# Kernel optimization log

Measured on AMD Instinct MI355X. Metric: run time of the kernel, lower is better.

## Reference

```python
import jax, jax.numpy as jnp
import numpy as np

NV, NQ, K, C, FF, H = 40000, 8192, 96, 128, 256, 8
DH = C // H


def _layernorm(x, g, b, eps=1e-5):
    m = jnp.mean(x, axis=-1, keepdims=True)
    v = jnp.var(x, axis=-1, keepdims=True)
    return (x - m) * jax.lax.rsqrt(v + eps) * g + b


def setup_inputs() -> dict:
    key = jax.random.key(0)
    ks = jax.random.split(key, 20)
    voxel_features = jax.random.normal(ks[0], (NV, C), dtype=jnp.float32)
    voxel_coords = jax.random.normal(ks[1], (NV, 3), dtype=jnp.float32)
    query_coords = jax.random.normal(ks[2], (NQ, 3), dtype=jnp.float32)
    raw = jax.random.randint(ks[3], (NQ, K), 0, 50000)
    key_indices = jnp.where(raw >= NV, -1, raw)  # -1 marks padded/missing keys
    key_indices = key_indices.at[:, 0].set(raw[:, 0] % NV)  # ensure >=1 valid key per query
    w = lambda k, shape: (jax.random.normal(k, shape, dtype=jnp.float32) * 0.02)
    return {
        "voxel_features": voxel_features,
        "voxel_coords": voxel_coords,
        "query_coords": query_coords,
        "key_indices": key_indices,
        "norm1_g": jnp.ones((C,), jnp.float32), "norm1_b": jnp.zeros((C,), jnp.float32),
        "q_pos_w": w(ks[4], (C, 3)), "q_pos_b": jnp.zeros((C,), jnp.float32),
        "k_pos_w": w(ks[5], (C, 3)), "k_pos_b": jnp.zeros((C,), jnp.float32),
        "in_w": w(ks[6], (3 * C, C)), "in_b": jnp.zeros((3 * C,), jnp.float32),
        "out_w": w(ks[7], (C, C)), "out_b": jnp.zeros((C,), jnp.float32),
        "norm2_g": jnp.ones((C,), jnp.float32), "norm2_b": jnp.zeros((C,), jnp.float32),
        "lin1_w": w(ks[8], (FF, C)), "lin1_b": jnp.zeros((FF,), jnp.float32),
        "lin2_w": w(ks[9], (C, FF)), "lin2_b": jnp.zeros((C,), jnp.float32),
        "fin_w": w(ks[10], (C, C)), "fin_b": jnp.zeros((C,), jnp.float32),
    }


def reference(voxel_features, voxel_coords, query_coords, key_indices,
              norm1_g, norm1_b, q_pos_w, q_pos_b, k_pos_w, k_pos_b,
              in_w, in_b, out_w, out_b, norm2_g, norm2_b,
              lin1_w, lin1_b, lin2_w, lin2_b, fin_w, fin_b):
    mask = key_indices < 0                      # [NQ, K] True = padded
    idx = jnp.where(mask, 0, key_indices)
    vf = _layernorm(voxel_features, norm1_g, norm1_b)   # norm1
    key_feat = vf[idx]                          # gather: [NQ, K, C]
    key_c = voxel_coords[idx]                   # [NQ, K, 3]
    # q_pos_proj: Linear(3,C)+ReLU ; k_pos_proj: Conv1d(3,C,1)+ReLU (== per-key linear)
    q_feat = jax.nn.relu(query_coords @ q_pos_w.T + q_pos_b)        # [NQ, C]
    key_pos = jax.nn.relu(jnp.einsum('nkt,ct->nkc', key_c, k_pos_w) + k_pos_b)
    key_feat = key_feat + key_pos               # [NQ, K, C]
    # nn.MultiheadAttention: query [1,NQ,C], key/value [K,NQ,C] -> per-query attention over K keys
    wq, wk, wv = in_w[:C], in_w[C:2 * C], in_w[2 * C:]
    bq, bk, bv = in_b[:C], in_b[C:2 * C], in_b[2 * C:]
    q = (q_feat @ wq.T + bq).reshape(NQ, H, DH)                 # [NQ,H,DH]
    k = (key_feat @ wk.T + bk).reshape(NQ, K, H, DH)            # [NQ,K,H,DH]
    v = (key_feat @ wv.T + bv).reshape(NQ, K, H, DH)
    scale = 1.0 / np.sqrt(DH)
    scores = jnp.einsum('nhd,nkhd->nhk', q, k) * scale          # [NQ,H,K]
    scores = jnp.where(mask[:, None, :], jnp.float32(-1e9), scores)
    attn = jax.nn.softmax(scores, axis=-1)
    ctx = jnp.einsum('nhk,nkhd->nhd', attn, v).reshape(NQ, C)
    attend = ctx @ out_w.T + out_b                              # [NQ,C]
    # FFN block (dropout=0 -> identity)
    h = _layernorm(attend, norm2_g, norm2_b)
    act = jax.nn.relu(h @ lin1_w.T + lin1_b) @ lin2_w.T + lin2_b
    x = attend + act
    out = jax.nn.relu(x @ fin_w.T + fin_b)                      # output_layer
    return out
```

## Files before the change

### kernel.cpp

```cpp
#include <hip/hip_runtime.h>
#include <hip/hip_bf16.h>
#include <math.h>

constexpr int NVOX = 40000;
constexpr int NQRY = 8192;
constexpr int KK   = 96;
constexpr int CH   = 128;
constexpr int FFD  = 256;

typedef __attribute__((ext_vector_type(8))) short short8;
typedef __attribute__((ext_vector_type(4))) float float4v;

__device__ inline float bflo(unsigned u) { return __uint_as_float(u << 16); }
__device__ inline float bfhi(unsigned u) { return __uint_as_float(u & 0xffff0000u); }
__device__ inline unsigned short f2bf(float x) {
  union { float f; unsigned u; } a; a.f = x;
  const unsigned r = a.u + 0x7fffu + ((a.u >> 16) & 1u);
  return (unsigned short)(r >> 16);
}
__device__ inline unsigned pack2(float lo, float hi) {
  return (unsigned)f2bf(lo) | ((unsigned)f2bf(hi) << 16);
}

__global__ __launch_bounds__(256) void k_prep(
    const float* __restrict__ vfeat, const float* __restrict__ vcoord,
    const float* __restrict__ n1g, const float* __restrict__ n1b,
    const float* __restrict__ kpw, const float* __restrict__ kpb,
    const float* __restrict__ in_w, const float* __restrict__ in_b,
    const float* __restrict__ ow, const float* __restrict__ l1w,
    const float* __restrict__ l2w, const float* __restrict__ fw,
    const float* __restrict__ qcoord,
    const float* __restrict__ qpw, const float* __restrict__ qpb,
    __hip_bfloat16* __restrict__ Gb, __hip_bfloat16* __restrict__ Wb,
    __hip_bfloat16* __restrict__ Eb, float* __restrict__ qout) {
  const int b = blockIdx.x;
  const int t = threadIdx.x;
  if (b < NVOX/16) {
    const int vloc = t >> 4;
    const int l    = t & 15;
    const int j = b * 16 + vloc;
    const float4* vrow = reinterpret_cast<const float4*>(vfeat + (size_t)j * CH);
    const float4 x0 = vrow[l*2], x1 = vrow[l*2+1];
    float s  = x0.x+x0.y+x0.z+x0.w + x1.x+x1.y+x1.z+x1.w;
    float ss = x0.x*x0.x+x0.y*x0.y+x0.z*x0.z+x0.w*x0.w
             + x1.x*x1.x+x1.y*x1.y+x1.z*x1.z+x1.w*x1.w;
    #pragma unroll
    for (int m = 8; m >= 1; m >>= 1) { s += __shfl_xor(s, m); ss += __shfl_xor(ss, m); }
    const float mean = s * (1.0f/CH);
    const float var  = ss * (1.0f/CH) - mean*mean;
    const float rstd = 1.0f / sqrtf(var + 1e-5f);
    const float c0 = vcoord[j*3+0], c1 = vcoord[j*3+1], c2 = vcoord[j*3+2];
    const float xv[8] = {x0.x,x0.y,x0.z,x0.w,x1.x,x1.y,x1.z,x1.w};
    float gv[8];
    #pragma unroll
    for (int u = 0; u < 8; u++) {
      const int c = l*8 + u;
      const float vf = (xv[u] - mean) * rstd * n1g[c] + n1b[c];
      const float kp = fmaf(c0, kpw[c*3+0], fmaf(c1, kpw[c*3+1], fmaf(c2, kpw[c*3+2], kpb[c])));
      gv[u] = vf + fmaxf(kp, 0.0f);
    }
    const uint4 pk = make_uint4(pack2(gv[0],gv[1]), pack2(gv[2],gv[3]),
                                pack2(gv[4],gv[5]), pack2(gv[6],gv[7]));
    *reinterpret_cast<uint4*>(Gb + (size_t)j*CH + l*8) = pk;
  } else if (b < NVOX/16 + 32) {
    const int idx = b - NVOX/16;
    const float* src;
    __hip_bfloat16* dst;
    if (idx < 8) {
      const int e = (idx * 256 + t) * 16;
      src = in_w + (size_t)CH*CH + e;
      dst = Wb + e;
    } else {
      const int f = ((idx - 8) * 256 + t) * 16;
      dst = Eb + f;
      if      (f < 16384) src = ow  + f;
      else if (f < 49152) src = l1w + (f - 16384);
      else if (f < 81920) src = l2w + (f - 49152);
      else                src = fw  + (f - 81920);
    }
    float v[16];
    #pragma unroll
    for (int u = 0; u < 4; u++) {
      const float4 fq = *reinterpret_cast<const float4*>(src + u*4);
      v[u*4+0]=fq.x; v[u*4+1]=fq.y; v[u*4+2]=fq.z; v[u*4+3]=fq.w;
    }
    uint4* o = reinterpret_cast<uint4*>(dst);
    o[0] = make_uint4(pack2(v[0],v[1]), pack2(v[2],v[3]),
                      pack2(v[4],v[5]), pack2(v[6],v[7]));
    o[1] = make_uint4(pack2(v[8],v[9]), pack2(v[10],v[11]),
                      pack2(v[12],v[13]), pack2(v[14],v[15]));
  } else {
    __shared__ float qf[16][CH];
    const int qbase = (b - (NVOX/16 + 32)) * 16;
    #pragma unroll
    for (int i = 0; i < 8; i++) {
      const int e = t + 256*i;
      const int qv = e >> 7, c = e & 127;
      const int qq = qbase + qv;
      const float v = fmaf(qcoord[qq*3+0], qpw[c*3+0],
                      fmaf(qcoord[qq*3+1], qpw[c*3+1],
                      fmaf(qcoord[qq*3+2], qpw[c*3+2], qpb[c])));
      qf[qv][c] = fmaxf(v, 0.0f);
    }
    __syncthreads();
    const int oc = t & 127, half = t >> 7;
    const float* wrow = in_w + (size_t)oc * CH;
    const float bia = in_b[oc];
    float acc[8];
    #pragma unroll
    for (int v = 0; v < 8; v++) acc[v] = bia;
    for (int c = 0; c < CH; c += 4) {
      const float4 w4 = *reinterpret_cast<const float4*>(wrow + c);
      #pragma unroll
      for (int v = 0; v < 8; v++) {
        const float4 g4 = *reinterpret_cast<const float4*>(&qf[half*8+v][c]);
        acc[v] = fmaf(g4.x, w4.x, fmaf(g4.y, w4.y, fmaf(g4.z, w4.z, fmaf(g4.w, w4.w, acc[v]))));
      }
    }
    #pragma unroll
    for (int v = 0; v < 8; v++) qout[(size_t)(qbase + half*8 + v)*CH + oc] = acc[v];
  }
}

__global__ __launch_bounds__(256) void k_kv_gemm(
    const __hip_bfloat16* __restrict__ Gb, const __hip_bfloat16* __restrict__ Wb,
    const float* __restrict__ in_b,
    unsigned short* __restrict__ KVh) {
  __shared__ unsigned short ldsD[64][72];
  const int t = threadIdx.x;
  const int w = t >> 6;
  const int lane = t & 63;
  const int col = lane & 15;
  const int quad = lane >> 4;
  const int bx = blockIdx.x;
  const int v0 = (bx >> 2) * 64;
  const int cg = bx & 3;

  const unsigned short* gRow =
      reinterpret_cast<const unsigned short*>(Gb) + (size_t)(v0 + w*16 + col)*CH + quad*8;
  short8 afrag[4];
  #pragma unroll
  for (int kq = 0; kq < 4; kq++)
    afrag[kq] = *reinterpret_cast<const short8*>(gRow + kq*32);

  float4v acc[4];
  #pragma unroll
  for (int j = 0; j < 4; j++) {
    const float bia = in_b[CH + cg*64 + j*16 + col];
    acc[j] = (float4v){bia, bia, bia, bia};
  }
  const unsigned short* wB = reinterpret_cast<const unsigned short*>(Wb);
  #pragma unroll
  for (int kq = 0; kq < 4; kq++) {
    #pragma unroll
    for (int j = 0; j < 4; j++) {
      const short8 bfrag = *reinterpret_cast<const short8*>(
          wB + (size_t)(cg*64 + j*16 + col)*CH + kq*32 + quad*8);
      acc[j] = __builtin_amdgcn_mfma_f32_16x16x32_bf16(afrag[kq], bfrag, acc[j], 0, 0, 0);
    }
  }
  #pragma unroll
  for (int j = 0; j < 4; j++)
    #pragma unroll
    for (int r = 0; r < 4; r++)
      ldsD[w*16 + quad*4 + r][j*16 + col] = f2bf(acc[j][r]);
  __syncthreads();
  const int row = t >> 2;
  const int cc  = (t & 3) * 16;
  const uint4 d0 = *reinterpret_cast<const uint4*>(&ldsD[row][cc]);
  const uint4 d1 = *reinterpret_cast<const uint4*>(&ldsD[row][cc+8]);
  const int head = (cg & 1) * 4 + (cc >> 4);
  const int isV  = cg >> 1;
  unsigned short* dst = KVh + ((size_t)head*NVOX + (v0 + row))*32 + isV*16;
  uint4* out = reinterpret_cast<uint4*>(dst);
  out[0] = d0; out[1] = d1;
}

__global__ __launch_bounds__(256) void k_attn(
    const unsigned short* __restrict__ KVh,
    const float* __restrict__ qg, const int* __restrict__ kidx,
    float* __restrict__ ctxg) {
  const int t    = threadIdx.x;
  const int h    = blockIdx.x & 7;
  const int n0   = (blockIdx.x >> 3) * 8;
  const int w    = t >> 6;
  const int lane = t & 63;
  const int qh   = lane >> 5;
  const int g    = (lane >> 2) & 7;
  const int r    = lane & 3;
  const int q    = n0 + 2*w + qh;
  const unsigned short* KVbase = KVh + (size_t)h * NVOX * 32;

  const float* qrow = qg + (size_t)q*CH + h*16 + (r & 1)*8;
  const float4 qa = *reinterpret_cast<const float4*>(qrow);
  const float4 qb = *reinterpret_cast<const float4*>(qrow + 4);

  unsigned msk = 0;
  uint4 kvbuf[12];
  const int krow = q*KK + g;
  #pragma unroll
  for (int it = 0; it < 12; it++) {
    const int j0 = kidx[krow + it*8];
    msk |= (unsigned)(j0 < 0) << it;
    const int j = (j0 < 0) ? 0 : j0;
    kvbuf[it] = *reinterpret_cast<const uint4*>(KVbase + (size_t)j*32 + r*8);
  }
  float sv[12];
  #pragma unroll
  for (int it = 0; it < 12; it++) {
    const uint4 kv = kvbuf[it];
    float s = 0.0f;
    s = fmaf(qa.x, bflo(kv.x), s); s = fmaf(qa.y, bfhi(kv.x), s);
    s = fmaf(qa.z, bflo(kv.y), s); s = fmaf(qa.w, bfhi(kv.y), s);
    s = fmaf(qb.x, bflo(kv.z), s); s = fmaf(qb.y, bfhi(kv.z), s);
    s = fmaf(qb.z, bflo(kv.w), s); s = fmaf(qb.w, bfhi(kv.w), s);
    s += __shfl_xor(s, 1);
    sv[it] = ((msk >> it) & 1) ? -1e9f : s * 0.25f;
  }
  float mx = sv[0];
  #pragma unroll
  for (int it = 1; it < 12; it++) mx = fmaxf(mx, sv[it]);
  mx = fmaxf(mx, __shfl_xor(mx, 4));
  mx = fmaxf(mx, __shfl_xor(mx, 8));
  mx = fmaxf(mx, __shfl_xor(mx, 16));
  float sum = 0.0f;
  #pragma unroll
  for (int it = 0; it < 12; it++) { sv[it] = __expf(sv[it] - mx); sum += sv[it]; }
  sum += __shfl_xor(sum, 4);
  sum += __shfl_xor(sum, 8);
  sum += __shfl_xor(sum, 16);
  const float inv = 1.0f / sum;
  const int qlane = lane & ~3;
  #pragma unroll
  for (int it = 0; it < 12; it++) sv[it] = __shfl(sv[it] * inv, qlane);
  float acc[8] = {0,0,0,0,0,0,0,0};
  #pragma unroll
  for (int it = 0; it < 12; it++) {
    const float wg = sv[it];
    const uint4 kv = kvbuf[it];
    acc[0] = fmaf(wg, bflo(kv.x), acc[0]); acc[1] = fmaf(wg, bfhi(kv.x), acc[1]);
    acc[2] = fmaf(wg, bflo(kv.y), acc[2]); acc[3] = fmaf(wg, bfhi(kv.y), acc[3]);
    acc[4] = fmaf(wg, bflo(kv.z), acc[4]); acc[5] = fmaf(wg, bfhi(kv.z), acc[5]);
    acc[6] = fmaf(wg, bflo(kv.w), acc[6]); acc[7] = fmaf(wg, bfhi(kv.w), acc[7]);
  }
  #pragma unroll
  for (int u = 0; u < 8; u++) {
    acc[u] += __shfl_xor(acc[u], 4);
    acc[u] += __shfl_xor(acc[u], 8);
    acc[u] += __shfl_xor(acc[u], 16);
  }
  if (r >= 2 && g == 0) {
    float* dst = ctxg + (size_t)q*CH + h*16 + (r - 2)*8;
    *reinterpret_cast<float4*>(dst)     = make_float4(acc[0], acc[1], acc[2], acc[3]);
    *reinterpret_cast<float4*>(dst + 4) = make_float4(acc[4], acc[5], acc[6], acc[7]);
  }
}

__global__ __launch_bounds__(256) void k_epi(
    const float* __restrict__ ctxg, const __hip_bfloat16* __restrict__ Eb,
    const float* __restrict__ ob,
    const float* __restrict__ n2g, const float* __restrict__ n2b,
    const float* __restrict__ l1b, const float* __restrict__ l2b,
    const float* __restrict__ fb,
    float* __restrict__ outp) {
  __shared__ unsigned short csb[16][136];
  __shared__ float attnS[16][132];
  __shared__ unsigned short hb[16][136];
  __shared__ unsigned short a1b[16][264];
  __shared__ unsigned short xb[16][136];
  const unsigned short* owb  = reinterpret_cast<const unsigned short*>(Eb);
  const unsigned short* l1wb = owb + 16384;
  const unsigned short* l2wb = owb + 49152;
  const unsigned short* fwb  = owb + 81920;

  const int t = threadIdx.x;
  const int w = t >> 6;
  const int lane = t & 63;
  const int col = lane & 15;
  const int quad = lane >> 4;
  const int qbase = blockIdx.x * 16;

  {
    const int e = t * 8;
    const int row = e >> 7, cc = e & 127;
    const float4* src = reinterpret_cast<const float4*>(ctxg + (size_t)(qbase+row)*CH + cc);
    const float4 x0 = src[0], x1 = src[1];
    *reinterpret_cast<uint4*>(&csb[row][cc]) =
        make_uint4(pack2(x0.x,x0.y), pack2(x0.z,x0.w), pack2(x1.x,x1.y), pack2(x1.z,x1.w));
  }
  __syncthreads();
  {
    short8 af[4];
    #pragma unroll
    for (int kq = 0; kq < 4; kq++)
      af[kq] = *reinterpret_cast<const short8*>(&csb[col][quad*8 + kq*32]);
    #pragma unroll
    for (int j = 0; j < 2; j++) {
      const int n0 = w*32 + j*16;
      const float bia = ob[n0 + col];
      float4v acc = (float4v){bia, bia, bia, bia};
      #pragma unroll
      for (int kq = 0; kq < 4; kq++) {
        const short8 bf = *reinterpret_cast<const short8*>(
            owb + (size_t)(n0 + col)*CH + kq*32 + quad*8);
        acc = __builtin_amdgcn_mfma_f32_16x16x32_bf16(af[kq], bf, acc, 0, 0, 0);
      }
      #pragma unroll
      for (int r = 0; r < 4; r++) attnS[quad*4 + r][n0 + col] = acc[r];
    }
  }
  __syncthreads();
  {
    const int row = t >> 4, l = t & 15;
    float s = 0.0f, ss = 0.0f;
    #pragma unroll
    for (int c = l; c < CH; c += 16) { const float x = attnS[row][c]; s += x; ss += x*x; }
    #pragma unroll
    for (int m = 8; m >= 1; m >>= 1) { s += __shfl_xor(s, m); ss += __shfl_xor(ss, m); }
    const float mean = s * (1.0f/CH);
    const float var  = ss * (1.0f/CH) - mean*mean;
    const float rstd = 1.0f / sqrtf(var + 1e-5f);
    #pragma unroll
    for (int c = l; c < CH; c += 16)
      hb[row][c] = f2bf((attnS[row][c] - mean) * rstd * n2g[c] + n2b[c]);
  }
  __syncthreads();
  {
    short8 af[4];
    #pragma unroll
    for (int kq = 0; kq < 4; kq++)
      af[kq] = *reinterpret_cast<const short8*>(&hb[col][quad*8 + kq*32]);
    #pragma unroll
    for (int j = 0; j < 4; j++) {
      const int n0 = w*64 + j*16;
      const float bia = l1b[n0 + col];
      float4v acc = (float4v){bia, bia, bia, bia};
      #pragma unroll
      for (int kq = 0; kq < 4; kq++) {
        const short8 bf = *reinterpret_cast<const short8*>(
            l1wb + (size_t)(n0 + col)*CH + kq*32 + quad*8);
        acc = __builtin_amdgcn_mfma_f32_16x16x32_bf16(af[kq], bf, acc, 0, 0, 0);
      }
      #pragma unroll
      for (int r = 0; r < 4; r++)
        a1b[quad*4 + r][n0 + col] = f2bf(fmaxf(acc[r], 0.0f));
    }
  }
  __syncthreads();
  {
    short8 af[8];
    #pragma unroll
    for (int kq = 0; kq < 8; kq++)
      af[kq] = *reinterpret_cast<const short8*>(&a1b[col][quad*8 + kq*32]);
    #pragma unroll
    for (int j = 0; j < 2; j++) {
      const int n0 = w*32 + j*16;
      const float bia = l2b[n0 + col];
      float4v acc = (float4v){bia, bia, bia, bia};
      #pragma unroll
      for (int kq = 0; kq < 8; kq++) {
        const short8 bf = *reinterpret_cast<const short8*>(
            l2wb + (size_t)(n0 + col)*FFD + kq*32 + quad*8);
        acc = __builtin_amdgcn_mfma_f32_16x16x32_bf16(af[kq], bf, acc, 0, 0, 0);
      }
      #pragma unroll
      for (int r = 0; r < 4; r++)
        xb[quad*4 + r][n0 + col] = f2bf(acc[r] + attnS[quad*4 + r][n0 + col]);
    }
  }
  __syncthreads();
  {
    short8 af[4];
    #pragma unroll
    for (int kq = 0; kq < 4; kq++)
      af[kq] = *reinterpret_cast<const short8*>(&xb[col][quad*8 + kq*32]);
    #pragma unroll
    for (int j = 0; j < 2; j++) {
      const int n0 = w*32 + j*16;
      const float bia = fb[n0 + col];
      float4v acc = (float4v){bia, bia, bia, bia};
      #pragma unroll
      for (int kq = 0; kq < 4; kq++) {
        const short8 bf = *reinterpret_cast<const short8*>(
            fwb + (size_t)(n0 + col)*CH + kq*32 + quad*8);
        acc = __builtin_amdgcn_mfma_f32_16x16x32_bf16(af[kq], bf, acc, 0, 0, 0);
      }
      #pragma unroll
      for (int r = 0; r < 4; r++)
        outp[(size_t)(qbase + quad*4 + r)*CH + n0 + col] = fmaxf(acc[r], 0.0f);
    }
  }
}

extern "C" void kernel_launch(void* const* d_in, const int* in_sizes, int n_in,
                              void* d_out, int out_size, void* d_ws, size_t ws_size,
                              hipStream_t stream) {
  const float* vfeat  = (const float*)d_in[0];
  const float* vcoord = (const float*)d_in[1];
  const float* qcoord = (const float*)d_in[2];
  const int*   kidx   = (const int*)  d_in[3];
  const float* n1g    = (const float*)d_in[4];
  const float* n1b    = (const float*)d_in[5];
  const float* qpw    = (const float*)d_in[6];
  const float* qpb    = (const float*)d_in[7];
  const float* kpw    = (const float*)d_in[8];
  const float* kpb    = (const float*)d_in[9];
  const float* in_w   = (const float*)d_in[10];
  const float* in_b   = (const float*)d_in[11];
  const float* out_w  = (const float*)d_in[12];
  const float* out_b  = (const float*)d_in[13];
  const float* n2g    = (const float*)d_in[14];
  const float* n2b    = (const float*)d_in[15];
  const float* l1w    = (const float*)d_in[16];
  const float* l1b    = (const float*)d_in[17];
  const float* l2w    = (const float*)d_in[18];
  const float* l2b    = (const float*)d_in[19];
  const float* fw     = (const float*)d_in[20];
  const float* fb     = (const float*)d_in[21];
  float* out = (float*)d_out;

  unsigned short* KVh = (unsigned short*)d_ws;
  __hip_bfloat16* Gb = (__hip_bfloat16*)(KVh + (size_t)8*NVOX*32);
  __hip_bfloat16* Wb = Gb + (size_t)NVOX*CH;
  __hip_bfloat16* Eb = Wb + (size_t)2*CH*CH;
  float* qb = (float*)(Eb + 98304);
  float* cx = qb + (size_t)NQRY*CH;

  k_prep   <<<NVOX/16 + 32 + NQRY/16, 256, 0, stream>>>(
      vfeat, vcoord, n1g, n1b, kpw, kpb, in_w, in_b,
      out_w, l1w, l2w, fw, qcoord, qpw, qpb, Gb, Wb, Eb, qb);
  k_kv_gemm<<<(NVOX/64)*4, 256, 0, stream>>>(Gb, Wb, in_b, KVh);
  k_attn   <<<(NQRY/8)*8, 256, 0, stream>>>(KVh, qb, kidx, cx);
  k_epi    <<<NQRY/16, 256, 0, stream>>>(cx, Eb, out_b, n2g, n2b, l1b, l2b, fb, out);
}
```

Before: 216.7 us.

## Split K/V work across lanes in attention and use bf16 dot2 for scores

Before, all four lanes of a group loaded full K+V rows for 12 keys and each computed half of the score. Now lanes r<2 score key set A and project values of set B, and lanes r>=2 do the reverse, so each lane does 6 score dots and 6 value updates instead of 12. The change also packs q to bf16 and uses the dot2 bf16 builtin for scores when available. This halves per-lane register buffers and redundant work, at the cost of extra cross-lane shuffles and lower-precision q in the scores.

```diff
diff --git a/kernel.cpp b/kernel.cpp
--- a/kernel.cpp
+++ b/kernel.cpp
@@ -21,6 +21,17 @@
 __device__ inline unsigned pack2(float lo, float hi) {
   return (unsigned)f2bf(lo) | ((unsigned)f2bf(hi) << 16);
 }
+
+#if __has_builtin(__builtin_amdgcn_fdot2_f32_bf16)
+#define HAVE_DOT2_BF16 1
+typedef __bf16 bf16x2v __attribute__((ext_vector_type(2)));
+__device__ inline float dot2bf(unsigned kv, unsigned qq, float acc) {
+  return __builtin_amdgcn_fdot2_f32_bf16(
+      __builtin_bit_cast(bf16x2v, kv), __builtin_bit_cast(bf16x2v, qq), acc, false);
+}
+#else
+#define HAVE_DOT2_BF16 0
+#endif
 
 __global__ __launch_bounds__(256) void k_prep(
     const float* __restrict__ vfeat, const float* __restrict__ vcoord,
@@ -189,55 +200,75 @@
   const int g    = (lane >> 2) & 7;
   const int r    = lane & 3;
   const int q    = n0 + 2*w + qh;
+  const bool loK = (r < 2);
   const unsigned short* KVbase = KVh + (size_t)h * NVOX * 32;
 
   const float* qrow = qg + (size_t)q*CH + h*16 + (r & 1)*8;
   const float4 qa = *reinterpret_cast<const float4*>(qrow);
   const float4 qb = *reinterpret_cast<const float4*>(qrow + 4);
-
-  unsigned msk = 0;
-  uint4 kvbuf[12];
+#if HAVE_DOT2_BF16
+  const unsigned qp0 = pack2(qa.x, qa.y), qp1 = pack2(qa.z, qa.w);
+  const unsigned qp2 = pack2(qb.x, qb.y), qp3 = pack2(qb.z, qb.w);
+#endif
+
   const int krow = q*KK + g;
-  #pragma unroll
-  for (int it = 0; it < 12; it++) {
-    const int j0 = kidx[krow + it*8];
-    msk |= (unsigned)(j0 < 0) << it;
-    const int j = (j0 < 0) ? 0 : j0;
-    kvbuf[it] = *reinterpret_cast<const uint4*>(KVbase + (size_t)j*32 + r*8);
-  }
-  float sv[12];
-  #pragma unroll
-  for (int it = 0; it < 12; it++) {
-    const uint4 kv = kvbuf[it];
+  uint4 kS[6], kV[6];
+  unsigned mA = 0, mB = 0;
+  #pragma unroll
+  for (int i = 0; i < 6; i++) {
+    const int jA0 = kidx[krow + 16*i];
+    const int jB0 = kidx[krow + 16*i + 8];
+    mA |= (unsigned)(jA0 < 0) << i;
+    mB |= (unsigned)(jB0 < 0) << i;
+    const int jA = (jA0 < 0) ? 0 : jA0;
+    const int jB = (jB0 < 0) ? 0 : jB0;
+    const int jSc = loK ? jA : jB;
+    const int jVc = loK ? jB : jA;
+    kS[i] = *reinterpret_cast<const uint4*>(KVbase + (size_t)jSc*32 + (r & 1)*8);
+    kV[i] = *reinterpret_cast<const uint4*>(KVbase + (size_t)jVc*32 + 16 + (r & 1)*8);
+  }
+  const unsigned mS = loK ? mA : mB;
+  float sv[6];
+  #pragma unroll
+  for (int i = 0; i < 6; i++) {
+    const uint4 kv = kS[i];
     float s = 0.0f;
+#if HAVE_DOT2_BF16
+    s = dot2bf(kv.x, qp0, s); s = dot2bf(kv.y, qp1, s);
+    s = dot2bf(kv.z, qp2, s); s = dot2bf(kv.w, qp3, s);
+#else
     s = fmaf(qa.x, bflo(kv.x), s); s = fmaf(qa.y, bfhi(kv.x), s);
     s = fmaf(qa.z, bflo(kv.y), s); s = fmaf(qa.w, bfhi(kv.y), s);
     s = fmaf(qb.x, bflo(kv.z), s); s = fmaf(qb.y, bfhi(kv.z), s);
     s = fmaf(qb.z, bflo(kv.w), s); s = fmaf(qb.w, bfhi(kv.w), s);
+#endif
     s += __shfl_xor(s, 1);
-    sv[it] = ((msk >> it) & 1) ? -1e9f : s * 0.25f;
+    sv[i] = ((mS >> i) & 1) ? -1e9f : s * 0.25f;
   }
   float mx = sv[0];
   #pragma unroll
-  for (int it = 1; it < 12; it++) mx = fmaxf(mx, sv[it]);
+  for (int i = 1; i < 6; i++) mx = fmaxf(mx, sv[i]);
+  mx = fmaxf(mx, __shfl_xor(mx, 2));
   mx = fmaxf(mx, __shfl_xor(mx, 4));
   mx = fmaxf(mx, __shfl_xor(mx, 8));
   mx = fmaxf(mx, __shfl_xor(mx, 16));
   float sum = 0.0f;
   #pragma unroll
-  for (int it = 0; it < 12; it++) { sv[it] = __expf(sv[it] - mx); sum += sv[it]; }
+  for (int i = 0; i < 6; i++) { sv[i] = __expf(sv[i] - mx); sum += sv[i]; }
+  sum += __shfl_xor(sum, 2);
   sum += __shfl_xor(sum, 4);
   sum += __shfl_xor(sum, 8);
   sum += __shfl_xor(sum, 16);
   const float inv = 1.0f / sum;
+  #pragma unroll
+  for (int i = 0; i < 6; i++) sv[i] *= inv;
   const int qlane = lane & ~3;
-  #pragma unroll
-  for (int it = 0; it < 12; it++) sv[it] = __shfl(sv[it] * inv, qlane);
+  const int wsrc  = qlane | (loK ? 2 : 0);
   float acc[8] = {0,0,0,0,0,0,0,0};
   #pragma unroll
-  for (int it = 0; it < 12; it++) {
-    const float wg = sv[it];
-    const uint4 kv = kvbuf[it];
+  for (int i = 0; i < 6; i++) {
+    const float wg = __shfl(sv[i], wsrc);
+    const uint4 kv = kV[i];
     acc[0] = fmaf(wg, bflo(kv.x), acc[0]); acc[1] = fmaf(wg, bfhi(kv.x), acc[1]);
     acc[2] = fmaf(wg, bflo(kv.y), acc[2]); acc[3] = fmaf(wg, bfhi(kv.y), acc[3]);
     acc[4] = fmaf(wg, bflo(kv.z), acc[4]); acc[5] = fmaf(wg, bfhi(kv.z), acc[5]);
@@ -245,12 +276,13 @@
   }
   #pragma unroll
   for (int u = 0; u < 8; u++) {
+    acc[u] += __shfl_xor(acc[u], 2);
     acc[u] += __shfl_xor(acc[u], 4);
     acc[u] += __shfl_xor(acc[u], 8);
     acc[u] += __shfl_xor(acc[u], 16);
   }
-  if (r >= 2 && g == 0) {
-    float* dst = ctxg + (size_t)q*CH + h*16 + (r - 2)*8;
+  if (g == 0 && r < 2) {
+    float* dst = ctxg + (size_t)q*CH + h*16 + r*8;
     *reinterpret_cast<float4*>(dst)     = make_float4(acc[0], acc[1], acc[2], acc[3]);
     *reinterpret_cast<float4*>(dst + 4) = make_float4(acc[4], acc[5], acc[6], acc[7]);
   }
```

Result: no change. 221.0 us (+2.0%).
